# Kernel tuning notes

Measured on AMD Instinct MI355X. Metric: run time of the kernel, lower is better.

Reference implementation:

```python
import jax, jax.numpy as jnp
import numpy as np

BAND_WIDTH = 0.5
EPS = 1e-5
NORM_EPS = 1e-12  # F.normalize eps


def setup_inputs() -> dict:
    key = jax.random.key(0)
    k1, k2 = jax.random.split(key)
    shape = (8, 512, 48, 48)  # N, C, H, W  (VGG conv4_4 features of a 384x384 image)
    return {
        "pred": jax.random.normal(k1, shape, dtype=jnp.float32),
        "target": jax.random.normal(k2, shape, dtype=jnp.float32),
    }


def reference(pred, target):
    N, C, H, W = pred.shape
    # center both by target channel-mean over (N, H, W)
    y_mu = jnp.mean(target, axis=(0, 2, 3), keepdims=True)
    x_c = pred - y_mu
    y_c = target - y_mu
    # L2-normalize along channel dim (F.normalize: divide by max(norm, eps))
    x_n = x_c / jnp.maximum(jnp.linalg.norm(x_c, axis=1, keepdims=True), NORM_EPS)
    y_n = y_c / jnp.maximum(jnp.linalg.norm(y_c, axis=1, keepdims=True), NORM_EPS)
    x_v = x_n.reshape(N, C, H * W)
    y_v = y_n.reshape(N, C, H * W)
    # pairwise cosine distance: [N, HW, HW]
    cosine_sim = jnp.einsum('ncp,ncq->npq', x_v, y_v)
    dist_raw = 1.0 - cosine_sim
    # relative distance: divide each row by its min over keys (dim=2)
    dist_min = jnp.min(dist_raw, axis=2, keepdims=True)
    dist_tilde = dist_raw / (dist_min + EPS)
    # similarity + row-normalize (softmax-like over dim=2)
    w = jnp.exp((1.0 - dist_tilde) / BAND_WIDTH)
    cx = w / jnp.sum(w, axis=2, keepdims=True)
    # max over query dim (dim=1), mean over key dim -> [N]
    cx = jnp.mean(jnp.max(cx, axis=1), axis=1)
    cx_loss = -jnp.log(cx + EPS)
    # reduction='mean', loss_weight=1.0
    return jnp.mean(cx_loss)
```

## Files before the change

kernel.cpp:

```cpp
#include <hip/hip_runtime.h>
#include <stdint.h>

#define NB 8
#define CC 512
#define PP 2304
#define EPSF 1e-5f
#define NTILES 648

typedef short bf16x8 __attribute__((ext_vector_type(8)));
typedef float f32x4 __attribute__((ext_vector_type(4)));

typedef __attribute__((address_space(3))) uint8_t lds8_t;
typedef __attribute__((address_space(1))) const uint8_t g8_t;

__device__ __forceinline__ void async16(void* lds, const void* g) {
  __builtin_amdgcn_global_load_lds((g8_t*)g, (lds8_t*)lds, 16, 0, 0);
}

__device__ __forceinline__ float bf2lo(uint32_t u) { return __uint_as_float(u << 16); }
__device__ __forceinline__ float bf2hi(uint32_t u) { return __uint_as_float(u & 0xffff0000u); }
__device__ __forceinline__ uint32_t f2bf(float f) {
  uint32_t u = __float_as_uint(f);
  return (u + 0x7fffu + ((u >> 16) & 1u)) >> 16;
}

template <int N>
__device__ __forceinline__ void vmwait() {
  if constexpr (N == 0) asm volatile("s_waitcnt vmcnt(0)" ::: "memory");
  else if constexpr (N == 2) asm volatile("s_waitcnt vmcnt(2)" ::: "memory");
  else if constexpr (N == 4) asm volatile("s_waitcnt vmcnt(4)" ::: "memory");
  else if constexpr (N == 6) asm volatile("s_waitcnt vmcnt(6)" ::: "memory");
}

__global__ __launch_bounds__(256) void k_cast(
    const float* __restrict__ pred, const float* __restrict__ tgt,
    uint16_t* __restrict__ xt, uint16_t* __restrict__ yt,
    float* __restrict__ ssx, float* __restrict__ ssy, float* __restrict__ musum) {
  __shared__ uint32_t lt[64][33];
  __shared__ float red[4][64];
  const int p0 = blockIdx.x * 64, c0 = blockIdx.y * 64, n = blockIdx.z;
  const int t = threadIdx.x, lp = t & 63, cb = t >> 6;
  for (int which = 0; which < 2; ++which) {
    const float* in = which ? tgt : pred;
    uint16_t* out = which ? yt : xt;
    float* ss = which ? ssy : ssx;
    float sq = 0.f;
    uint32_t packs[8];
#pragma unroll
    for (int i = 0; i < 16; ++i) {
      const int c = c0 + cb * 16 + i;
      float v = in[((size_t)n * CC + c) * PP + p0 + lp];
      sq += v * v;
      uint32_t b = f2bf(v);
      if (i & 1) packs[i >> 1] |= b << 16; else packs[i >> 1] = b;
    }
#pragma unroll
    for (int j = 0; j < 8; ++j) lt[lp][cb * 8 + j] = packs[j];
    red[cb][lp] = sq;
    __syncthreads();
    if (t < 64)
      atomicAdd(&ss[(size_t)n * PP + p0 + t],
                red[0][t] + red[1][t] + red[2][t] + red[3][t]);
    if (which && t < 32) {
      float s0 = 0.f, s1 = 0.f;
      for (int p = 0; p < 64; ++p) {
        const uint32_t u = lt[p][t];
        s0 += bf2lo(u); s1 += bf2hi(u);
      }
      atomicAdd(&musum[c0 + 2 * t], s0);
      atomicAdd(&musum[c0 + 2 * t + 1], s1);
    }
    const int p = t >> 2, ch = t & 3;
    uint4 v0, v1;
    v0.x = lt[p][ch * 8 + 0]; v0.y = lt[p][ch * 8 + 1];
    v0.z = lt[p][ch * 8 + 2]; v0.w = lt[p][ch * 8 + 3];
    v1.x = lt[p][ch * 8 + 4]; v1.y = lt[p][ch * 8 + 5];
    v1.z = lt[p][ch * 8 + 6]; v1.w = lt[p][ch * 8 + 7];
    uint4* ob = (uint4*)(out + (((size_t)n * PP + p0 + p) * CC + c0 + ch * 16));
    ob[0] = v0; ob[1] = v1;
    __syncthreads();
  }
}

__global__ __launch_bounds__(256) void k_gemv(
    const float* __restrict__ musum,
    const uint16_t* __restrict__ xt, const uint16_t* __restrict__ yt,
    float* __restrict__ mvx, float* __restrict__ mvy) {
  const uint16_t* T = blockIdx.y ? yt : xt;
  float* mv = blockIdx.y ? mvy : mvx;
  __shared__ float mu_l[512];
  __shared__ float m2red[4];
  const int t = threadIdx.x, w = t >> 6, lane = t & 63;
  const float scale = 1.0f / (NB * PP);
  float m2p = 0.f;
  for (int i = t; i < 512; i += 256) {
    float m = musum[i] * scale;
    mu_l[i] = m;
    m2p += m * m;
  }
#pragma unroll
  for (int d = 1; d < 64; d <<= 1) m2p += __shfl_xor(m2p, d);
  if (lane == 0) m2red[w] = m2p;
  __syncthreads();
  const float mu2h = 0.5f * (m2red[0] + m2red[1] + m2red[2] + m2red[3]);
  for (int it = 0; it < 16; ++it) {
    const int r = blockIdx.x * 64 + w * 16 + it;
    uint4 u = *(const uint4*)(T + (size_t)r * CC + lane * 8);
    float s = 0.f;
    const float* m = &mu_l[lane * 8];
    s += bf2lo(u.x) * m[0] + bf2hi(u.x) * m[1];
    s += bf2lo(u.y) * m[2] + bf2hi(u.y) * m[3];
    s += bf2lo(u.z) * m[4] + bf2hi(u.z) * m[5];
    s += bf2lo(u.w) * m[6] + bf2hi(u.w) * m[7];
#pragma unroll
    for (int d = 1; d < 64; d <<= 1) s += __shfl_xor(s, d);
    if (lane == 0) mv[r] = s - mu2h;
  }
}

__device__ __forceinline__ void stage_half(uint16_t* dst, const uint16_t* g, int tid) {
  async16((char*)dst + tid * 16, g);
  async16((char*)dst + tid * 16 + 8192, g + 64 * CC);
}

template <int QM, int QN, bool LA, bool LB, int VM>
__device__ __forceinline__ void phase(const uint16_t (*R)[8192],
                                      uint16_t* d1, const uint16_t* s1,
                                      uint16_t* d2, const uint16_t* s2,
                                      int tid, int lane, int wr, int wcn,
                                      bf16x8 (&af)[4][2], bf16x8 (&bfv)[2][2],
                                      f32x4 (&acc)[2][4][2][2]) {
  if (LA) {
#pragma unroll
    for (int i = 0; i < 4; ++i) {
      const int rh = wr * 64 + i * 16 + (lane & 15);
      const char* base = (const char*)R[QM] + rh * 128;
      const int sw = (rh & 7) << 4;
#pragma unroll
      for (int kk = 0; kk < 2; ++kk)
        af[i][kk] = *(const bf16x8*)(base + ((kk * 64 + (lane >> 4) * 16) ^ sw));
    }
  }
  if (LB) {
#pragma unroll
    for (int j = 0; j < 2; ++j) {
      const int rh = wcn * 32 + j * 16 + (lane & 15);
      const char* base = (const char*)R[2 + QN] + rh * 128;
      const int sw = (rh & 7) << 4;
#pragma unroll
      for (int kk = 0; kk < 2; ++kk)
        bfv[j][kk] = *(const bf16x8*)(base + ((kk * 64 + (lane >> 4) * 16) ^ sw));
    }
  }
  if (d1) stage_half(d1, s1, tid);
  if (d2) stage_half(d2, s2, tid);
  __builtin_amdgcn_s_barrier();
  asm volatile("s_waitcnt lgkmcnt(0)" ::: "memory");
  __builtin_amdgcn_s_setprio(1);
#pragma unroll
  for (int i = 0; i < 4; ++i)
#pragma unroll
    for (int j = 0; j < 2; ++j)
#pragma unroll
      for (int kk = 0; kk < 2; ++kk)
        acc[QM][i][QN][j] = __builtin_amdgcn_mfma_f32_16x16x32_bf16(
            af[i][kk], bfv[j][kk], acc[QM][i][QN][j], 0, 0, 0);
  __builtin_amdgcn_s_setprio(0);
  vmwait<VM>();
  __builtin_amdgcn_s_barrier();
}

__global__ __launch_bounds__(512, 2) void k_gemm(
    const uint16_t* __restrict__ xt, const uint16_t* __restrict__ yt,
    const float* __restrict__ ssx, const float* __restrict__ ssy,
    const float* __restrict__ mvx, const float* __restrict__ mvy,
    uint16_t* __restrict__ S, int* __restrict__ ctr) {
  __shared__ uint16_t lds[2][4][8192];
  __shared__ int tshare;
  const int tid = threadIdx.x, lane = tid & 63, wid = tid >> 6;
  const int wr = wid >> 2, wcn = wid & 3;

  for (;;) {
    if (tid == 0) tshare = atomicAdd(ctr, 1);
    __syncthreads();
    const int flat = tshare;
    __syncthreads();
    if (flat >= NTILES) return;
    const int nb = flat / 81;
    const int rem = flat - nb * 81;
    const int m0 = (rem % 9) * 256, n0 = (rem / 9) * 256;
    const uint16_t* Ax = xt + (size_t)nb * PP * CC;
    const uint16_t* By = yt + (size_t)nb * PP * CC;
    const int lswz = (tid & 7) ^ ((tid >> 3) & 7);
    const uint16_t* gAb = Ax + (size_t)(m0 + (tid >> 3)) * CC + lswz * 8;
    const uint16_t* gBb = By + (size_t)(n0 + (tid >> 3)) * CC + lswz * 8;

    f32x4 acc[2][4][2][2];
#pragma unroll
    for (int a = 0; a < 2; ++a)
#pragma unroll
      for (int b = 0; b < 4; ++b)
#pragma unroll
        for (int c = 0; c < 2; ++c)
#pragma unroll
          for (int d = 0; d < 2; ++d) acc[a][b][c][d] = (f32x4){0.f, 0.f, 0.f, 0.f};

    stage_half(lds[0][0], gAb, tid);
    stage_half(lds[0][2], gBb, tid);
    stage_half(lds[0][1], gAb + 128 * CC, tid);
    stage_half(lds[0][3], gBb + 128 * CC, tid);
    stage_half(lds[1][0], gAb + 64, tid);
    vmwait<6>();
    __builtin_amdgcn_s_barrier();

    bf16x8 af[4][2], bfv[2][2];
    for (int kt = 0; kt < 6; ++kt) {
      const uint16_t(*R)[8192] = lds[kt & 1];
      uint16_t(*Wn)[8192] = lds[(kt & 1) ^ 1];
      uint16_t(*Wc)[8192] = lds[kt & 1];
      const int ko1 = (kt + 1) * 64, ko2 = (kt + 2) * 64;
      phase<0, 0, true, true, 6>(R, Wn[1], gAb + 128 * CC + ko1, Wn[2], gBb + ko1,
                                 tid, lane, wr, wcn, af, bfv, acc);
      phase<0, 1, false, true, -1>(R, Wn[3], gBb + 128 * CC + ko1, nullptr, nullptr,
                                   tid, lane, wr, wcn, af, bfv, acc);
      phase<1, 1, true, false, -1>(R, Wc[0], gAb + ko2, nullptr, nullptr,
                                   tid, lane, wr, wcn, af, bfv, acc);
      phase<1, 0, false, true, 4>(R, nullptr, nullptr, nullptr, nullptr,
                                  tid, lane, wr, wcn, af, bfv, acc);
    }
    {
      const uint16_t(*R)[8192] = lds[0];
      phase<0, 0, true, true, 6>(R, lds[1][1], gAb + 128 * CC + 7 * 64,
                                 lds[1][2], gBb + 7 * 64, tid, lane, wr, wcn, af, bfv, acc);
      phase<0, 1, false, true, -1>(R, lds[1][3], gBb + 128 * CC + 7 * 64, nullptr, nullptr,
                                   tid, lane, wr, wcn, af, bfv, acc);
      phase<1, 1, true, false, -1>(R, nullptr, nullptr, nullptr, nullptr,
                                   tid, lane, wr, wcn, af, bfv, acc);
      phase<1, 0, false, true, 2>(R, nullptr, nullptr, nullptr, nullptr,
                                  tid, lane, wr, wcn, af, bfv, acc);
    }
    {
      const uint16_t(*R)[8192] = lds[1];
      phase<0, 0, true, true, 0>(R, nullptr, nullptr, nullptr, nullptr,
                                 tid, lane, wr, wcn, af, bfv, acc);
      phase<0, 1, false, true, -1>(R, nullptr, nullptr, nullptr, nullptr,
                                   tid, lane, wr, wcn, af, bfv, acc);
      phase<1, 1, true, false, -1>(R, nullptr, nullptr, nullptr, nullptr,
                                   tid, lane, wr, wcn, af, bfv, acc);
      phase<1, 0, false, true, -1>(R, nullptr, nullptr, nullptr, nullptr,
                                   tid, lane, wr, wcn, af, bfv, acc);
    }

    const float* rsp = ssx + (size_t)nb * PP + m0;
    const float* csp = ssy + (size_t)nb * PP + n0;
    const float* mvr = mvx + (size_t)nb * PP + m0;
    const float* mvc = mvy + (size_t)nb * PP + n0;
    uint16_t* Sp = S + (size_t)nb * PP * PP;
    float cinv[2][2], cmv[2][2];
#pragma unroll
    for (int qn = 0; qn < 2; ++qn)
#pragma unroll
      for (int j = 0; j < 2; ++j) {
        const int col = qn * 128 + wcn * 32 + j * 16 + (lane & 15);
        const float m = mvc[col];
        cmv[qn][j] = m;
        cinv[qn][j] = 1.0f / fmaxf(sqrtf(csp[col] - 2.0f * m), 1e-12f);
      }
#pragma unroll
    for (int qm = 0; qm < 2; ++qm)
#pragma unroll
      for (int i = 0; i < 4; ++i)
#pragma unroll
        for (int r = 0; r < 4; ++r) {
          const int row = qm * 128 + wr * 64 + i * 16 + (lane >> 4) * 4 + r;
          const float mr = mvr[row];
          const float rinv = 1.0f / fmaxf(sqrtf(rsp[row] - 2.0f * mr), 1e-12f);
          uint16_t* orow = Sp + (size_t)(m0 + row) * PP + n0;
#pragma unroll
          for (int qn = 0; qn < 2; ++qn)
#pragma unroll
            for (int j = 0; j < 2; ++j)
              orow[qn * 128 + wcn * 32 + j * 16 + (lane & 15)] = (uint16_t)f2bf(
                  (acc[qm][i][qn][j][r] - mr - cmv[qn][j]) * rinv * cinv[qn][j]);
        }
  }
}

__global__ __launch_bounds__(256) void k_rowcol(const uint16_t* __restrict__ S,
                                                int* __restrict__ cxcol) {
  const int pc = blockIdx.x, n = blockIdx.y;
  __shared__ float lsc[24], lb[24], lri[24];
  const int t = threadIdx.x, w = t >> 6, lane = t & 63;
  const size_t Sn = (size_t)n * PP * PP;
  for (int it = 0; it < 6; ++it) {
    const int r = w * 6 + it;
    const uint2* rp = (const uint2*)(S + Sn + (size_t)(pc * 24 + r) * PP);
    uint2 u[9];
#pragma unroll
    for (int k = 0; k < 9; ++k) u[k] = rp[lane + k * 64];
    float v[36];
#pragma unroll
    for (int k = 0; k < 9; ++k) {
      v[4 * k + 0] = bf2lo(u[k].x);
      v[4 * k + 1] = bf2hi(u[k].x);
      v[4 * k + 2] = bf2lo(u[k].y);
      v[4 * k + 3] = bf2hi(u[k].y);
    }
    float mx = v[0];
#pragma unroll
    for (int k = 1; k < 36; ++k) mx = fmaxf(mx, v[k]);
#pragma unroll
    for (int d = 1; d < 64; d <<= 1) mx = fmaxf(mx, __shfl_xor(mx, d));
    const float sc = 2.0f / (1.0f - mx + EPSF);
    const float b = (EPSF - mx) * sc;
    float s = 0.f;
#pragma unroll
    for (int k = 0; k < 36; ++k) s += __expf(fmaf(v[k], sc, b));
#pragma unroll
    for (int d = 1; d < 64; d <<= 1) s += __shfl_xor(s, d);
    if (lane == 0) { lsc[r] = sc; lb[r] = b; lri[r] = 1.0f / s; }
  }
  __syncthreads();
  const uint32_t* Sc = (const uint32_t*)(S + Sn + (size_t)(pc * 24) * PP);
  for (int pi = t; pi < PP / 2; pi += 256) {
    float b0 = 0.f, b1 = 0.f;
#pragma unroll
    for (int r = 0; r < 24; ++r) {
      const uint32_t u = Sc[(size_t)r * (PP / 2) + pi];
      b0 = fmaxf(b0, __expf(fmaf(bf2lo(u), lsc[r], lb[r])) * lri[r]);
      b1 = fmaxf(b1, __expf(fmaf(bf2hi(u), lsc[r], lb[r])) * lri[r]);
    }
    atomicMax(&cxcol[n * PP + 2 * pi], __float_as_int(b0));
    atomicMax(&cxcol[n * PP + 2 * pi + 1], __float_as_int(b1));
  }
}

__global__ __launch_bounds__(512) void k_fin(const int* __restrict__ cxcol,
                                             float* __restrict__ out) {
  __shared__ float red[8];
  const int t = threadIdx.x, w = t >> 6, lane = t & 63;
  float s = 0.f;
  for (int q = lane; q < PP; q += 64) s += __int_as_float(cxcol[w * PP + q]);
#pragma unroll
  for (int d = 1; d < 64; d <<= 1) s += __shfl_xor(s, d);
  if (lane == 0) red[w] = -logf(s * (1.0f / PP) + EPSF);
  __syncthreads();
  if (t == 0) {
    float a = 0.f;
#pragma unroll
    for (int n = 0; n < NB; ++n) a += red[n];
    out[0] = a * (1.0f / NB);
  }
}

extern "C" void kernel_launch(void* const* d_in, const int* in_sizes, int n_in,
                              void* d_out, int out_size, void* d_ws, size_t ws_size,
                              hipStream_t stream) {
  const float* pred = (const float*)d_in[0];
  const float* tgt  = (const float*)d_in[1];
  float* W = (float*)d_ws;
  float* musum = W + 0;
  float* ssx   = W + 512;
  float* ssy   = W + 18944;
  int*   cxcol = (int*)(W + 37376);
  int*   ctr   = (int*)(W + 55808);
  float* mvx   = W + 56320;
  float* mvy   = W + 74752;
  uint16_t* xt = (uint16_t*)(W + 93440);
  uint16_t* yt = xt + (size_t)NB * PP * CC;
  uint16_t* S  = yt + (size_t)NB * PP * CC;

  hipMemsetAsync(W, 0, 55812 * sizeof(float), stream);

  k_cast<<<dim3(PP / 64, CC / 64, NB), dim3(256), 0, stream>>>(
      pred, tgt, xt, yt, ssx, ssy, musum);
  k_gemv<<<dim3(288, 2), dim3(256), 0, stream>>>(musum, xt, yt, mvx, mvy);
  k_gemm<<<dim3(256), dim3(512), 0, stream>>>(xt, yt, ssx, ssy, mvx, mvy, S, ctr);
  k_rowcol<<<dim3(96, NB), dim3(256), 0, stream>>>(S, cxcol);
  k_fin<<<dim3(1), dim3(512), 0, stream>>>(cxcol, (float*)d_out);
}
```

Measured before the change: 166.4 us.

## Static GEMM grid with retuned prefetch schedule; cache exp weights in LDS for rowcol

The GEMM drops the atomic work-stealing loop and launches one block per tile on a 9x9xN grid, with a remap meant to spread batches across XCDs. It also reworks the K-loop so every phase reloads B fragments and issues one staging copy, with deeper prefetch. The row/column kernel now computes the exp weights once per row, stores them as bf16 in LDS, and takes the column max from LDS in two 12-row halves. This avoids recomputing exp and rereading S from global memory, at the cost of extra bf16 rounding of the weights and more LDS traffic.

```diff
diff --git a/kernel.cpp b/kernel.cpp
--- a/kernel.cpp
+++ b/kernel.cpp
@@ -5,7 +5,7 @@
 #define CC 512
 #define PP 2304
 #define EPSF 1e-5f
-#define NTILES 648
+#define RCH 12
 
 typedef short bf16x8 __attribute__((ext_vector_type(8)));
 typedef float f32x4 __attribute__((ext_vector_type(4)));
@@ -27,9 +27,9 @@
 template <int N>
 __device__ __forceinline__ void vmwait() {
   if constexpr (N == 0) asm volatile("s_waitcnt vmcnt(0)" ::: "memory");
-  else if constexpr (N == 2) asm volatile("s_waitcnt vmcnt(2)" ::: "memory");
   else if constexpr (N == 4) asm volatile("s_waitcnt vmcnt(4)" ::: "memory");
   else if constexpr (N == 6) asm volatile("s_waitcnt vmcnt(6)" ::: "memory");
+  else if constexpr (N == 8) asm volatile("s_waitcnt vmcnt(8)" ::: "memory");
 }
 
 __global__ __launch_bounds__(256) void k_cast(
@@ -123,13 +123,11 @@
   async16((char*)dst + tid * 16 + 8192, g + 64 * CC);
 }
 
-template <int QM, int QN, bool LA, bool LB, int VM>
+template <int QM, int QN, bool LA, bool STG, int VM>
 __device__ __forceinline__ void phase(const uint16_t (*R)[8192],
-                                      uint16_t* d1, const uint16_t* s1,
-                                      uint16_t* d2, const uint16_t* s2,
+                                      uint16_t* sdst, const uint16_t* ssrc,
                                       int tid, int lane, int wr, int wcn,
-                                      bf16x8 (&af)[4][2], bf16x8 (&bfv)[2][2],
-                                      f32x4 (&acc)[2][4][2][2]) {
+                                      bf16x8 (&af)[4][2], f32x4 (&acc)[2][4][2][2]) {
   if (LA) {
 #pragma unroll
     for (int i = 0; i < 4; ++i) {
@@ -141,19 +139,17 @@
         af[i][kk] = *(const bf16x8*)(base + ((kk * 64 + (lane >> 4) * 16) ^ sw));
     }
   }
-  if (LB) {
-#pragma unroll
-    for (int j = 0; j < 2; ++j) {
-      const int rh = wcn * 32 + j * 16 + (lane & 15);
-      const char* base = (const char*)R[2 + QN] + rh * 128;
-      const int sw = (rh & 7) << 4;
-#pragma unroll
-      for (int kk = 0; kk < 2; ++kk)
-        bfv[j][kk] = *(const bf16x8*)(base + ((kk * 64 + (lane >> 4) * 16) ^ sw));
-    }
-  }
-  if (d1) stage_half(d1, s1, tid);
-  if (d2) stage_half(d2, s2, tid);
+  bf16x8 bfv[2][2];
+#pragma unroll
+  for (int j = 0; j < 2; ++j) {
+    const int rh = wcn * 32 + j * 16 + (lane & 15);
+    const char* base = (const char*)R[2 + QN] + rh * 128;
+    const int sw = (rh & 7) << 4;
+#pragma unroll
+    for (int kk = 0; kk < 2; ++kk)
+      bfv[j][kk] = *(const bf16x8*)(base + ((kk * 64 + (lane >> 4) * 16) ^ sw));
+  }
+  if (STG) stage_half(sdst, ssrc, tid);
   __builtin_amdgcn_s_barrier();
   asm volatile("s_waitcnt lgkmcnt(0)" ::: "memory");
   __builtin_amdgcn_s_setprio(1);
@@ -174,164 +170,173 @@
     const uint16_t* __restrict__ xt, const uint16_t* __restrict__ yt,
     const float* __restrict__ ssx, const float* __restrict__ ssy,
     const float* __restrict__ mvx, const float* __restrict__ mvy,
-    uint16_t* __restrict__ S, int* __restrict__ ctr) {
+    uint16_t* __restrict__ S) {
   __shared__ uint16_t lds[2][4][8192];
-  __shared__ int tshare;
+  int flat = blockIdx.x + 9 * blockIdx.y + 81 * blockIdx.z;
+  flat = (flat & 7) * 81 + (flat >> 3);
+  const int nb = flat / 81;
+  const int rem = flat - nb * 81;
+  const int m0 = (rem % 9) * 256, n0 = (rem / 9) * 256;
   const int tid = threadIdx.x, lane = tid & 63, wid = tid >> 6;
   const int wr = wid >> 2, wcn = wid & 3;
-
-  for (;;) {
-    if (tid == 0) tshare = atomicAdd(ctr, 1);
-    __syncthreads();
-    const int flat = tshare;
-    __syncthreads();
-    if (flat >= NTILES) return;
-    const int nb = flat / 81;
-    const int rem = flat - nb * 81;
-    const int m0 = (rem % 9) * 256, n0 = (rem / 9) * 256;
-    const uint16_t* Ax = xt + (size_t)nb * PP * CC;
-    const uint16_t* By = yt + (size_t)nb * PP * CC;
-    const int lswz = (tid & 7) ^ ((tid >> 3) & 7);
-    const uint16_t* gAb = Ax + (size_t)(m0 + (tid >> 3)) * CC + lswz * 8;
-    const uint16_t* gBb = By + (size_t)(n0 + (tid >> 3)) * CC + lswz * 8;
-
-    f32x4 acc[2][4][2][2];
-#pragma unroll
-    for (int a = 0; a < 2; ++a)
-#pragma unroll
-      for (int b = 0; b < 4; ++b)
-#pragma unroll
-        for (int c = 0; c < 2; ++c)
-#pragma unroll
-          for (int d = 0; d < 2; ++d) acc[a][b][c][d] = (f32x4){0.f, 0.f, 0.f, 0.f};
-
-    stage_half(lds[0][0], gAb, tid);
-    stage_half(lds[0][2], gBb, tid);
-    stage_half(lds[0][1], gAb + 128 * CC, tid);
-    stage_half(lds[0][3], gBb + 128 * CC, tid);
-    stage_half(lds[1][0], gAb + 64, tid);
-    vmwait<6>();
-    __builtin_amdgcn_s_barrier();
-
-    bf16x8 af[4][2], bfv[2][2];
-    for (int kt = 0; kt < 6; ++kt) {
-      const uint16_t(*R)[8192] = lds[kt & 1];
-      uint16_t(*Wn)[8192] = lds[(kt & 1) ^ 1];
-      uint16_t(*Wc)[8192] = lds[kt & 1];
-      const int ko1 = (kt + 1) * 64, ko2 = (kt + 2) * 64;
-      phase<0, 0, true, true, 6>(R, Wn[1], gAb + 128 * CC + ko1, Wn[2], gBb + ko1,
-                                 tid, lane, wr, wcn, af, bfv, acc);
-      phase<0, 1, false, true, -1>(R, Wn[3], gBb + 128 * CC + ko1, nullptr, nullptr,
-                                   tid, lane, wr, wcn, af, bfv, acc);
-      phase<1, 1, true, false, -1>(R, Wc[0], gAb + ko2, nullptr, nullptr,
-                                   tid, lane, wr, wcn, af, bfv, acc);
-      phase<1, 0, false, true, 4>(R, nullptr, nullptr, nullptr, nullptr,
-                                  tid, lane, wr, wcn, af, bfv, acc);
-    }
-    {
-      const uint16_t(*R)[8192] = lds[0];
-      phase<0, 0, true, true, 6>(R, lds[1][1], gAb + 128 * CC + 7 * 64,
-                                 lds[1][2], gBb + 7 * 64, tid, lane, wr, wcn, af, bfv, acc);
-      phase<0, 1, false, true, -1>(R, lds[1][3], gBb + 128 * CC + 7 * 64, nullptr, nullptr,
-                                   tid, lane, wr, wcn, af, bfv, acc);
-      phase<1, 1, true, false, -1>(R, nullptr, nullptr, nullptr, nullptr,
-                                   tid, lane, wr, wcn, af, bfv, acc);
-      phase<1, 0, false, true, 2>(R, nullptr, nullptr, nullptr, nullptr,
-                                  tid, lane, wr, wcn, af, bfv, acc);
-    }
-    {
-      const uint16_t(*R)[8192] = lds[1];
-      phase<0, 0, true, true, 0>(R, nullptr, nullptr, nullptr, nullptr,
-                                 tid, lane, wr, wcn, af, bfv, acc);
-      phase<0, 1, false, true, -1>(R, nullptr, nullptr, nullptr, nullptr,
-                                   tid, lane, wr, wcn, af, bfv, acc);
-      phase<1, 1, true, false, -1>(R, nullptr, nullptr, nullptr, nullptr,
-                                   tid, lane, wr, wcn, af, bfv, acc);
-      phase<1, 0, false, true, -1>(R, nullptr, nullptr, nullptr, nullptr,
-                                   tid, lane, wr, wcn, af, bfv, acc);
-    }
-
-    const float* rsp = ssx + (size_t)nb * PP + m0;
-    const float* csp = ssy + (size_t)nb * PP + n0;
-    const float* mvr = mvx + (size_t)nb * PP + m0;
-    const float* mvc = mvy + (size_t)nb * PP + n0;
-    uint16_t* Sp = S + (size_t)nb * PP * PP;
-    float cinv[2][2], cmv[2][2];
-#pragma unroll
-    for (int qn = 0; qn < 2; ++qn)
-#pragma unroll
-      for (int j = 0; j < 2; ++j) {
-        const int col = qn * 128 + wcn * 32 + j * 16 + (lane & 15);
-        const float m = mvc[col];
-        cmv[qn][j] = m;
-        cinv[qn][j] = 1.0f / fmaxf(sqrtf(csp[col] - 2.0f * m), 1e-12f);
-      }
-#pragma unroll
-    for (int qm = 0; qm < 2; ++qm)
-#pragma unroll
-      for (int i = 0; i < 4; ++i)
-#pragma unroll
-        for (int r = 0; r < 4; ++r) {
-          const int row = qm * 128 + wr * 64 + i * 16 + (lane >> 4) * 4 + r;
-          const float mr = mvr[row];
-          const float rinv = 1.0f / fmaxf(sqrtf(rsp[row] - 2.0f * mr), 1e-12f);
-          uint16_t* orow = Sp + (size_t)(m0 + row) * PP + n0;
-#pragma unroll
-          for (int qn = 0; qn < 2; ++qn)
-#pragma unroll
-            for (int j = 0; j < 2; ++j)
-              orow[qn * 128 + wcn * 32 + j * 16 + (lane & 15)] = (uint16_t)f2bf(
-                  (acc[qm][i][qn][j][r] - mr - cmv[qn][j]) * rinv * cinv[qn][j]);
-        }
-  }
+  const uint16_t* Ax = xt + (size_t)nb * PP * CC;
+  const uint16_t* By = yt + (size_t)nb * PP * CC;
+  const int lswz = (tid & 7) ^ ((tid >> 3) & 7);
+  const uint16_t* gAb = Ax + (size_t)(m0 + (tid >> 3)) * CC + lswz * 8;
+  const uint16_t* gBb = By + (size_t)(n0 + (tid >> 3)) * CC + lswz * 8;
+
+  f32x4 acc[2][4][2][2];
+#pragma unroll
+  for (int a = 0; a < 2; ++a)
+#pragma unroll
+    for (int b = 0; b < 4; ++b)
+#pragma unroll
+      for (int c = 0; c < 2; ++c)
+#pragma unroll
+        for (int d = 0; d < 2; ++d) acc[a][b][c][d] = (f32x4){0.f, 0.f, 0.f, 0.f};
+
+  stage_half(lds[0][0], gAb, tid);
+  stage_half(lds[0][2], gBb, tid);
+  stage_half(lds[0][1], gAb + 128 * CC, tid);
+  stage_half(lds[0][3], gBb + 128 * CC, tid);
+  stage_half(lds[1][0], gAb + 64, tid);
+  stage_half(lds[1][2], gBb + 64, tid);
+  vmwait<8>();
+  __builtin_amdgcn_s_barrier();
+
+  bf16x8 af[4][2];
+  for (int kt = 0; kt < 6; ++kt) {
+    const int cur = kt & 1;
+    const uint16_t(*R)[8192] = lds[cur];
+    uint16_t(*Wn)[8192] = lds[cur ^ 1];
+    uint16_t(*Wc)[8192] = lds[cur];
+    const int ko = (kt + 1) * 64;
+    phase<0, 0, true, true, 6>(R, Wn[1], gAb + 128 * CC + ko, tid, lane, wr, wcn, af, acc);
+    phase<0, 1, false, true, -1>(R, Wn[3], gBb + 128 * CC + ko, tid, lane, wr, wcn, af, acc);
+    phase<1, 0, true, true, -1>(R, Wc[0], gAb + ko + 64, tid, lane, wr, wcn, af, acc);
+    phase<1, 1, false, true, 8>(R, Wc[2], gBb + ko + 64, tid, lane, wr, wcn, af, acc);
+  }
+  {
+    const uint16_t(*R)[8192] = lds[0];
+    phase<0, 0, true, true, 6>(R, lds[1][1], gAb + 128 * CC + 7 * 64, tid, lane, wr, wcn, af, acc);
+    phase<0, 1, false, true, -1>(R, lds[1][3], gBb + 128 * CC + 7 * 64, tid, lane, wr, wcn, af, acc);
+    phase<1, 0, true, false, -1>(R, nullptr, nullptr, tid, lane, wr, wcn, af, acc);
+    phase<1, 1, false, false, 4>(R, nullptr, nullptr, tid, lane, wr, wcn, af, acc);
+  }
+  {
+    const uint16_t(*R)[8192] = lds[1];
+    phase<0, 0, true, false, 0>(R, nullptr, nullptr, tid, lane, wr, wcn, af, acc);
+    phase<0, 1, false, false, -1>(R, nullptr, nullptr, tid, lane, wr, wcn, af, acc);
+    phase<1, 0, true, false, -1>(R, nullptr, nullptr, tid, lane, wr, wcn, af, acc);
+    phase<1, 1, false, false, -1>(R, nullptr, nullptr, tid, lane, wr, wcn, af, acc);
+  }
+
+  const float* rsp = ssx + (size_t)nb * PP + m0;
+  const float* csp = ssy + (size_t)nb * PP + n0;
+  const float* mvr = mvx + (size_t)nb * PP + m0;
+  const float* mvc = mvy + (size_t)nb * PP + n0;
+  uint16_t* Sp = S + (size_t)nb * PP * PP;
+  float cinv[2][2], cmv[2][2];
+#pragma unroll
+  for (int qn = 0; qn < 2; ++qn)
+#pragma unroll
+    for (int j = 0; j < 2; ++j) {
+      const int col = qn * 128 + wcn * 32 + j * 16 + (lane & 15);
+      const float m = mvc[col];
+      cmv[qn][j] = m;
+      cinv[qn][j] = 1.0f / fmaxf(sqrtf(csp[col] - 2.0f * m), 1e-12f);
+    }
+#pragma unroll
+  for (int qm = 0; qm < 2; ++qm)
+#pragma unroll
+    for (int i = 0; i < 4; ++i)
+#pragma unroll
+      for (int r = 0; r < 4; ++r) {
+        const int row = qm * 128 + wr * 64 + i * 16 + (lane >> 4) * 4 + r;
+        const float mr = mvr[row];
+        const float rinv = 1.0f / fmaxf(sqrtf(rsp[row] - 2.0f * mr), 1e-12f);
+        uint16_t* orow = Sp + (size_t)(m0 + row) * PP + n0;
+#pragma unroll
+        for (int qn = 0; qn < 2; ++qn)
+#pragma unroll
+          for (int j = 0; j < 2; ++j)
+            orow[qn * 128 + wcn * 32 + j * 16 + (lane & 15)] = (uint16_t)f2bf(
+                (acc[qm][i][qn][j][r] - mr - cmv[qn][j]) * rinv * cinv[qn][j]);
+      }
 }
 
 __global__ __launch_bounds__(256) void k_rowcol(const uint16_t* __restrict__ S,
                                                 int* __restrict__ cxcol) {
   const int pc = blockIdx.x, n = blockIdx.y;
-  __shared__ float lsc[24], lb[24], lri[24];
+  __shared__ uint16_t wlds[RCH][PP];
+  __shared__ float lri[RCH];
   const int t = threadIdx.x, w = t >> 6, lane = t & 63;
-  const size_t Sn = (size_t)n * PP * PP;
-  for (int it = 0; it < 6; ++it) {
-    const int r = w * 6 + it;
-    const uint2* rp = (const uint2*)(S + Sn + (size_t)(pc * 24 + r) * PP);
-    uint2 u[9];
-#pragma unroll
-    for (int k = 0; k < 9; ++k) u[k] = rp[lane + k * 64];
-    float v[36];
-#pragma unroll
-    for (int k = 0; k < 9; ++k) {
-      v[4 * k + 0] = bf2lo(u[k].x);
-      v[4 * k + 1] = bf2hi(u[k].x);
-      v[4 * k + 2] = bf2lo(u[k].y);
-      v[4 * k + 3] = bf2hi(u[k].y);
-    }
-    float mx = v[0];
-#pragma unroll
-    for (int k = 1; k < 36; ++k) mx = fmaxf(mx, v[k]);
-#pragma unroll
-    for (int d = 1; d < 64; d <<= 1) mx = fmaxf(mx, __shfl_xor(mx, d));
-    const float sc = 2.0f / (1.0f - mx + EPSF);
-    const float b = (EPSF - mx) * sc;
-    float s = 0.f;
-#pragma unroll
-    for (int k = 0; k < 36; ++k) s += __expf(fmaf(v[k], sc, b));
-#pragma unroll
-    for (int d = 1; d < 64; d <<= 1) s += __shfl_xor(s, d);
-    if (lane == 0) { lsc[r] = sc; lb[r] = b; lri[r] = 1.0f / s; }
-  }
-  __syncthreads();
-  const uint32_t* Sc = (const uint32_t*)(S + Sn + (size_t)(pc * 24) * PP);
-  for (int pi = t; pi < PP / 2; pi += 256) {
-    float b0 = 0.f, b1 = 0.f;
-#pragma unroll
-    for (int r = 0; r < 24; ++r) {
-      const uint32_t u = Sc[(size_t)r * (PP / 2) + pi];
-      b0 = fmaxf(b0, __expf(fmaf(bf2lo(u), lsc[r], lb[r])) * lri[r]);
-      b1 = fmaxf(b1, __expf(fmaf(bf2hi(u), lsc[r], lb[r])) * lri[r]);
-    }
-    atomicMax(&cxcol[n * PP + 2 * pi], __float_as_int(b0));
-    atomicMax(&cxcol[n * PP + 2 * pi + 1], __float_as_int(b1));
+  const size_t Sn = (size_t)n * PP * PP + (size_t)pc * 24 * PP;
+  float best0[5], best1[5];
+#pragma unroll
+  for (int i = 0; i < 5; ++i) { best0[i] = 0.f; best1[i] = 0.f; }
+  for (int half = 0; half < 2; ++half) {
+    for (int it = 0; it < 3; ++it) {
+      const int r = w * 3 + it;
+      const uint2* rp = (const uint2*)(S + Sn + (size_t)(half * RCH + r) * PP);
+      uint2 u[9];
+#pragma unroll
+      for (int k = 0; k < 9; ++k) u[k] = rp[lane + k * 64];
+      float v[36];
+#pragma unroll
+      for (int k = 0; k < 9; ++k) {
+        v[4 * k + 0] = bf2lo(u[k].x); v[4 * k + 1] = bf2hi(u[k].x);
+        v[4 * k + 2] = bf2lo(u[k].y); v[4 * k + 3] = bf2hi(u[k].y);
+      }
+      float mx = v[0];
+#pragma unroll
+      for (int k = 1; k < 36; ++k) mx = fmaxf(mx, v[k]);
+#pragma unroll
+      for (int d = 1; d < 64; d <<= 1) mx = fmaxf(mx, __shfl_xor(mx, d));
+      const float sc = 2.0f / (1.0f - mx + EPSF);
+      const float b = (EPSF - mx) * sc;
+      float s = 0.f;
+#pragma unroll
+      for (int k = 0; k < 9; ++k) {
+        const float w0 = __expf(fmaf(v[4 * k + 0], sc, b));
+        const float w1 = __expf(fmaf(v[4 * k + 1], sc, b));
+        const float w2 = __expf(fmaf(v[4 * k + 2], sc, b));
+        const float w3 = __expf(fmaf(v[4 * k + 3], sc, b));
+        s += (w0 + w1) + (w2 + w3);
+        uint2 wp;
+        wp.x = f2bf(w0) | (f2bf(w1) << 16);
+        wp.y = f2bf(w2) | (f2bf(w3) << 16);
+        ((uint2*)&wlds[r][0])[lane + k * 64] = wp;
+      }
+#pragma unroll
+      for (int d = 1; d < 64; d <<= 1) s += __shfl_xor(s, d);
+      if (lane == 0) lri[r] = 1.0f / s;
+    }
+    __syncthreads();
+#pragma unroll
+    for (int i = 0; i < 5; ++i) {
+      const int pi = t + i * 256;
+      if (pi < PP / 2) {
+        float b0 = best0[i], b1 = best1[i];
+#pragma unroll
+        for (int r = 0; r < RCH; ++r) {
+          const uint32_t u = ((const uint32_t*)&wlds[r][0])[pi];
+          const float ri = lri[r];
+          b0 = fmaxf(b0, bf2lo(u) * ri);
+          b1 = fmaxf(b1, bf2hi(u) * ri);
+        }
+        best0[i] = b0; best1[i] = b1;
+      }
+    }
+    __syncthreads();
+  }
+#pragma unroll
+  for (int i = 0; i < 5; ++i) {
+    const int pi = t + i * 256;
+    if (pi < PP / 2) {
+      atomicMax(&cxcol[n * PP + 2 * pi], __float_as_int(best0[i]));
+      atomicMax(&cxcol[n * PP + 2 * pi + 1], __float_as_int(best1[i]));
+    }
   }
 }
 
@@ -363,19 +368,18 @@
   float* ssx   = W + 512;
   float* ssy   = W + 18944;
   int*   cxcol = (int*)(W + 37376);
-  int*   ctr   = (int*)(W + 55808);
   float* mvx   = W + 56320;
   float* mvy   = W + 74752;
   uint16_t* xt = (uint16_t*)(W + 93440);
   uint16_t* yt = xt + (size_t)NB * PP * CC;
   uint16_t* S  = yt + (size_t)NB * PP * CC;
 
-  hipMemsetAsync(W, 0, 55812 * sizeof(float), stream);
+  hipMemsetAsync(W, 0, 55808 * sizeof(float), stream);
 
   k_cast<<<dim3(PP / 64, CC / 64, NB), dim3(256), 0, stream>>>(
       pred, tgt, xt, yt, ssx, ssy, musum);
   k_gemv<<<dim3(288, 2), dim3(256), 0, stream>>>(musum, xt, yt, mvx, mvy);
-  k_gemm<<<dim3(256), dim3(512), 0, stream>>>(xt, yt, ssx, ssy, mvx, mvy, S, ctr);
+  k_gemm<<<dim3(9, 9, NB), dim3(512), 0, stream>>>(xt, yt, ssx, ssy, mvx, mvy, S);
   k_rowcol<<<dim3(96, NB), dim3(256), 0, stream>>>(S, cxcol);
   k_fin<<<dim3(1), dim3(512), 0, stream>>>(cxcol, (float*)d_out);
 }
```

New measurement: 158.8 us. 4.6% less time.
